# Kernel optimization log

Hardware: AMD Instinct MI355X
Metric: run time of the kernel (lower is better)

## Reference

```python
import jax, jax.numpy as jnp
import numpy as np

N_NODES = 100000
N_EDGES = 1600000
IN_SIZE, HID_SIZE, OUT_SIZE = 128, 64, 64


def _glorot(key, shape):
    lim = float(np.sqrt(6.0 / (shape[0] + shape[1])))
    return jax.random.uniform(key, shape, jnp.float32, -lim, lim)


def setup_inputs() -> dict:
    key = jax.random.key(0)
    ks = jax.random.split(key, 6)
    features = jax.random.normal(ks[0], (N_NODES, IN_SIZE), jnp.float32)
    src = jax.random.randint(ks[1], (N_EDGES,), 0, N_NODES)
    dst = jax.random.randint(ks[2], (N_EDGES,), 0, N_NODES)
    return {
        "features": features,
        "W0": _glorot(ks[3], (IN_SIZE, HID_SIZE)),
        "b0": jnp.zeros((HID_SIZE,), jnp.float32),
        "W1": _glorot(ks[4], (HID_SIZE, HID_SIZE)),
        "b1": jnp.zeros((HID_SIZE,), jnp.float32),
        "W2": _glorot(ks[5], (HID_SIZE, OUT_SIZE)),
        "b2": jnp.zeros((OUT_SIZE,), jnp.float32),
        "src": src,
        "dst": dst,
    }


def reference(features, W0, b0, W1, b1, W2, b2, src, dst):
    # DGL GraphConv with norm='both': h' = relu(D_in^{-1/2} A D_out^{-1/2} h W + b)
    # Dropout layers are identity in eval mode (deterministic baseline).
    N = features.shape[0]
    ones = jnp.ones(src.shape, features.dtype)
    deg_out = jax.ops.segment_sum(ones, src, num_segments=N)
    deg_in = jax.ops.segment_sum(ones, dst, num_segments=N)
    norm_src = jnp.where(deg_out > 0, deg_out, 1.0) ** -0.5  # [N]
    norm_dst = jnp.where(deg_in > 0, deg_in, 1.0) ** -0.5    # [N]

    def layer(h, W, b):
        h = h * norm_src[:, None]          # source-side degree norm
        m = (h @ W)[src]                   # project first (in >= out), then gather [E, d_out]
        agg = jax.ops.segment_sum(m, dst, num_segments=N)  # scatter-add to destinations
        return jax.nn.relu(agg * norm_dst[:, None] + b)

    h = layer(features, W0, b0)
    h = layer(h, W1, b1)
    return layer(h, W2, b2)
```

## Files before the change

### kernel.cpp

```cpp
#include <hip/hip_runtime.h>
#include <hip/hip_bf16.h>

typedef __hip_bfloat16 bf16;
typedef __attribute__((ext_vector_type(8))) short bf16x8;
typedef __attribute__((ext_vector_type(8))) unsigned short u16x8;
typedef __attribute__((ext_vector_type(4))) float f32x4;
typedef __attribute__((ext_vector_type(4))) int i32x4;
typedef __attribute__((ext_vector_type(4))) short s16x4;

__device__ __forceinline__ float b2f(unsigned short u) {
  return __uint_as_float(((unsigned)u) << 16);
}
__device__ __forceinline__ unsigned short f2b(float x) {
  bf16 h = __float2bfloat16(x);
  return *reinterpret_cast<unsigned short*>(&h);
}

__global__ void k_passA(const int* __restrict__ src, const int* __restrict__ dst, int E,
                        int nbuck, int M, int* __restrict__ counts,
                        const unsigned short* __restrict__ raw, int* __restrict__ flag) {
  if (blockIdx.x == 256) {
    __shared__ int sbad, snz;
    const int t = threadIdx.x;
    if (t == 0) { sbad = 0; snz = 0; }
    __syncthreads();
    const unsigned short u = raw[t];
    const float a = fabsf(b2f(u));
    if (!(a < 100.f)) atomicAdd(&sbad, 1);
    if (((t & 1) == 0) && u != 0) atomicAdd(&snz, 1);
    __syncthreads();
    if (t == 0) flag[0] = (sbad == 0 && snz > 0) ? 1 : 0;
    return;
  }
  extern __shared__ int lh[];
  int* lh1 = lh;
  int* lh2 = lh + nbuck;
  const int t = threadIdx.x;
  for (int k = t; k < 2 * nbuck; k += 256) lh[k] = 0;
  __syncthreads();
  const int chunk = (E + 255) / 256;
  const int s = blockIdx.x * chunk;
  const int e = min(E, s + chunk);
  for (int i = s + t; i < e; i += 256) {
    atomicAdd(&lh1[dst[i] >> 8], 1);
    atomicAdd(&lh2[src[i] >> 8], 1);
  }
  __syncthreads();
  for (int k = t; k < nbuck; k += 256) {
    counts[k * 256 + blockIdx.x] = lh1[k];
    counts[M + k * 256 + blockIdx.x] = lh2[k];
  }
}

__global__ void k_scan1(const int* __restrict__ a, int M2, int* __restrict__ bsums) {
  __shared__ int sdata[256];
  int i = blockIdx.x * 256 + threadIdx.x;
  int v = (i < M2) ? a[i] : 0;
  sdata[threadIdx.x] = v;
  __syncthreads();
  for (int s = 128; s > 0; s >>= 1) {
    if (threadIdx.x < s) sdata[threadIdx.x] += sdata[threadIdx.x + s];
    __syncthreads();
  }
  if (threadIdx.x == 0) bsums[blockIdx.x] = sdata[0];
}

__global__ void k_scan2(int* __restrict__ bsums, int nb, int* __restrict__ rowStart,
                        int N, int E) {
  __shared__ int s[1024];
  const int t = threadIdx.x;
  const int v = (t < nb) ? bsums[t] : 0;
  s[t] = v;
  __syncthreads();
  for (int off = 1; off < 1024; off <<= 1) {
    int u = (t >= off) ? s[t - off] : 0;
    __syncthreads();
    s[t] += u;
    __syncthreads();
  }
  if (t < nb) bsums[t] = s[t] - v;
  if (t == 0) rowStart[N] = E;
}

__global__ void k_scan3(int* __restrict__ a, int M2, const int* __restrict__ bsums) {
  __shared__ int sdata[256];
  int i = blockIdx.x * 256 + threadIdx.x;
  int v = (i < M2) ? a[i] : 0;
  sdata[threadIdx.x] = v;
  __syncthreads();
  for (int off = 1; off < 256; off <<= 1) {
    int t = (threadIdx.x >= off) ? sdata[threadIdx.x - off] : 0;
    __syncthreads();
    sdata[threadIdx.x] += t;
    __syncthreads();
  }
  if (i < M2) a[i] = bsums[blockIdx.x] + sdata[threadIdx.x] - v;
}

__global__ void k_passC(const int* __restrict__ src, const int* __restrict__ dst, int E,
                        int nbuck, int M, const int* __restrict__ S,
                        int* __restrict__ tmp, unsigned char* __restrict__ tmp2) {
  extern __shared__ int cur[];
  int* cur1 = cur;
  int* cur2 = cur + nbuck;
  const int t = threadIdx.x;
  for (int k = t; k < nbuck; k += 256) {
    cur1[k] = S[k * 256 + blockIdx.x];
    cur2[k] = S[M + k * 256 + blockIdx.x];
  }
  __syncthreads();
  const int chunk = (E + 255) / 256;
  const int s = blockIdx.x * chunk;
  const int e = min(E, s + chunk);
  for (int i = s + t; i < e; i += 256) {
    const int sv = src[i];
    const int d = dst[i];
    const int pos1 = atomicAdd(&cur1[d >> 8], 1);
    tmp[pos1] = sv | ((d & 255) << 20);
    const int pos2 = atomicAdd(&cur2[sv >> 8], 1);
    tmp2[pos2 - E] = (unsigned char)(sv & 255);
  }
}

__global__ void k_passD(const int* __restrict__ tmp, const unsigned char* __restrict__ tmp2,
                        const int* __restrict__ S, int nbuck, int M, int N, int E,
                        int* __restrict__ rowStart, int* __restrict__ edgeSrc,
                        float* __restrict__ ns, float* __restrict__ nd) {
  __shared__ int h[256];
  __shared__ int ex[256];
  __shared__ int c[256];
  const int t = threadIdx.x;
  const int k = blockIdx.x;
  const int node = k * 256 + t;
  const int bs2 = S[M + k * 256] - E;
  const int be2 = (k + 1 < nbuck) ? (S[M + (k + 1) * 256] - E) : E;
  h[t] = 0;
  __syncthreads();
  for (int i = bs2 + t; i < be2; i += 256) atomicAdd(&h[tmp2[i]], 1);
  __syncthreads();
  if (node < N) {
    int dov = h[t];
    if (dov <= 0) dov = 1;
    ns[node] = rsqrtf((float)dov);
  }
  __syncthreads();
  const int bs = S[k * 256];
  const int be = (k + 1 < nbuck) ? S[(k + 1) * 256] : E;
  h[t] = 0;
  __syncthreads();
  for (int i = bs + t; i < be; i += 256) atomicAdd(&h[tmp[i] >> 20], 1);
  __syncthreads();
  const int cnt = h[t];
  ex[t] = cnt;
  __syncthreads();
  for (int off = 1; off < 256; off <<= 1) {
    int u = (t >= off) ? ex[t - off] : 0;
    __syncthreads();
    ex[t] += u;
    __syncthreads();
  }
  const int excl = ex[t] - cnt;
  if (node < N) {
    rowStart[node] = bs + excl;
    nd[node] = rsqrtf((float)(cnt > 0 ? cnt : 1));
  }
  c[t] = bs + excl;
  __syncthreads();
  for (int i = bs + t; i < be; i += 256) {
    const int v = tmp[i];
    const int pos = atomicAdd(&c[v >> 20], 1);
    edgeSrc[pos] = v & 0xFFFFF;
  }
}

template <int K, bool FIRST, bool SCALE>
__device__ __forceinline__ void gemm_loadA(const void* hin, bool isb, int rowA,
                                           int quad, bf16x8* A) {
  constexpr int KT = K / 32;
  if (FIRST && !isb) {
    const float* hp = (const float*)hin + (size_t)rowA * K;
#pragma unroll
    for (int kt = 0; kt < KT; ++kt) {
      const float4 u0 = *(const float4*)(hp + kt * 32 + quad * 8);
      const float4 u1 = *(const float4*)(hp + kt * 32 + quad * 8 + 4);
      A[kt][0] = (short)f2b(u0.x); A[kt][1] = (short)f2b(u0.y);
      A[kt][2] = (short)f2b(u0.z); A[kt][3] = (short)f2b(u0.w);
      A[kt][4] = (short)f2b(u1.x); A[kt][5] = (short)f2b(u1.y);
      A[kt][6] = (short)f2b(u1.z); A[kt][7] = (short)f2b(u1.w);
    }
  } else {
    const unsigned short* hp = (const unsigned short*)hin + (size_t)rowA * K;
#pragma unroll
    for (int kt = 0; kt < KT; ++kt)
      A[kt] = *(const bf16x8*)(hp + kt * 32 + quad * 8);
  }
}

template <int K, bool FIRST, bool SCALE>
__global__ void __launch_bounds__(256) k_gemm(
    const void* __restrict__ hin, const void* __restrict__ Wv,
    const int* __restrict__ flag, const float* __restrict__ norm_src,
    int N, unsigned short* __restrict__ out) {
  constexpr int KT = K / 32;
  constexpr int ST = K + 8;
  constexpr int CST = 72;
  __shared__ unsigned short Wl[64 * ST];
  __shared__ unsigned short Cl[4][16 * CST];
  const bool isb = (*flag != 0);
  const int tid = threadIdx.x;

  {
    const unsigned short* Wus = (const unsigned short*)Wv;
    const float* Wf = (const float*)Wv;
    for (int i0 = tid * 8; i0 < K * 64; i0 += 2048) {
      const int k = i0 >> 6;
      const int n0 = i0 & 63;
      unsigned short v[8];
      if (isb) {
        const u16x8 u = *(const u16x8*)(Wus + i0);
#pragma unroll
        for (int j = 0; j < 8; ++j) v[j] = u[j];
      } else {
        const float4 f0 = *(const float4*)(Wf + i0);
        const float4 f1 = *(const float4*)(Wf + i0 + 4);
        v[0] = f2b(f0.x); v[1] = f2b(f0.y); v[2] = f2b(f0.z); v[3] = f2b(f0.w);
        v[4] = f2b(f1.x); v[5] = f2b(f1.y); v[6] = f2b(f1.z); v[7] = f2b(f1.w);
      }
#pragma unroll
      for (int j = 0; j < 8; ++j) Wl[(n0 + j) * ST + k] = v[j];
    }
  }
  __syncthreads();

  const int lane = tid & 63;
  const int quad = lane >> 4;
  const int l16 = lane & 15;
  const int w = tid >> 6;
  unsigned short* myC = &Cl[w][0];

  const int wid = blockIdx.x * 4 + w;
  const int nw = gridDim.x * 4;
  const int G = (N + 15) >> 4;

  bf16x8 A0[KT], A1[KT];
  if (wid < G) {
    int r0 = (wid << 4) + l16;
    if (r0 >= N) r0 = N - 1;
    gemm_loadA<K, FIRST, SCALE>(hin, isb, r0, quad, A0);
  }
  for (int g = wid; g < G; g += nw) {
    if (g + nw < G) {
      int r1 = ((g + nw) << 4) + l16;
      if (r1 >= N) r1 = N - 1;
      gemm_loadA<K, FIRST, SCALE>(hin, isb, r1, quad, A1);
    }
    f32x4 acc[4] = {{0.f, 0.f, 0.f, 0.f}, {0.f, 0.f, 0.f, 0.f},
                    {0.f, 0.f, 0.f, 0.f}, {0.f, 0.f, 0.f, 0.f}};
#pragma unroll
    for (int kt = 0; kt < KT; ++kt) {
      const int koff = kt * 32 + quad * 8;
#pragma unroll
      for (int nt = 0; nt < 4; ++nt) {
        const bf16x8 Bf = *(const bf16x8*)&Wl[(nt * 16 + l16) * ST + koff];
        acc[nt] = __builtin_amdgcn_mfma_f32_16x16x32_bf16(A0[kt], Bf, acc[nt], 0, 0, 0);
      }
    }
    const int rowD = quad * 4;
#pragma unroll
    for (int r = 0; r < 4; ++r) {
      const int nodeW = (g << 4) + rowD + r;
      const float f = (SCALE && nodeW < N) ? norm_src[nodeW] : 1.0f;
#pragma unroll
      for (int nt = 0; nt < 4; ++nt)
        myC[(rowD + r) * CST + nt * 16 + l16] = f2b(SCALE ? acc[nt][r] * f : acc[nt][r]);
    }
    const int row2 = lane >> 2;
    const int c0 = (lane & 3) * 16;
    const int node = (g << 4) + row2;
    if (node < N) {
      const u16x8 v0 = *(const u16x8*)&myC[row2 * CST + c0];
      const u16x8 v1 = *(const u16x8*)&myC[row2 * CST + c0 + 8];
      *(u16x8*)(out + (size_t)node * 64 + c0) = v0;
      *(u16x8*)(out + (size_t)node * 64 + c0 + 8) = v1;
    }
#pragma unroll
    for (int kt = 0; kt < KT; ++kt) A0[kt] = A1[kt];
  }
}

__device__ __forceinline__ void agg_chunk_compute(unsigned trbase, int cb32, int lo,
                                                  unsigned span, int quad, f32x4* acc) {
  const int posbase = cb32 + (quad << 2);
  const unsigned u0 = (unsigned)(posbase - lo);
  bf16x8 Af;
#pragma unroll
  for (int j = 0; j < 8; ++j) {
    const unsigned off = (j < 4) ? (unsigned)j : (unsigned)(12 + j);
    Af[j] = ((u0 + off) < span) ? (short)0x3F80 : (short)0;
  }
  s16x4 t0[4], t1[4];
#pragma unroll
  for (int nt = 0; nt < 4; ++nt) {
    const unsigned a = trbase + (unsigned)(nt * 1024);
    asm volatile("ds_read_b64_tr_b16 %0, %1" : "=v"(t0[nt]) : "v"(a) : "memory");
    asm volatile("ds_read_b64_tr_b16 %0, %1 offset:512" : "=v"(t1[nt]) : "v"(a) : "memory");
  }
  asm volatile("s_waitcnt lgkmcnt(0)" ::: "memory");
  __builtin_amdgcn_sched_barrier(0);
#pragma unroll
  for (int nt = 0; nt < 4; ++nt) {
    bf16x8 Bf;
    Bf[0] = t0[nt][0]; Bf[1] = t0[nt][1]; Bf[2] = t0[nt][2]; Bf[3] = t0[nt][3];
    Bf[4] = t1[nt][0]; Bf[5] = t1[nt][1]; Bf[6] = t1[nt][2]; Bf[7] = t1[nt][3];
    acc[nt] = __builtin_amdgcn_mfma_f32_16x16x32_bf16(Af, Bf, acc[nt], 0, 0, 0);
  }
}

template <bool LAST, bool FUSE>
__global__ void __launch_bounds__(256) k_aggregate(
    const unsigned short* __restrict__ proj,
    const int* __restrict__ edgeSrc, const int* __restrict__ rowStart,
    const float* __restrict__ norm_dst, const float* __restrict__ norm_src,
    const void* __restrict__ bias, const int* __restrict__ flag,
    const void* __restrict__ Wv, int N, int E, void* __restrict__ outp) {
  __shared__ unsigned short lds[4][2048];
  const bool isb = (*flag != 0);
  const int tid = threadIdx.x;
  const int w = tid >> 6;
  const int lane = tid & 63;
  const int l16 = lane & 15;
  const int quad = lane >> 4;
  const int e32 = lane & 31;
  const int p = lane >> 5;

  const int wid = blockIdx.x * 4 + w;
  const int g0 = wid * 8;

  float bcol[4];
#pragma unroll
  for (int nt = 0; nt < 4; ++nt) {
    const int col = nt * 16 + l16;
    bcol[nt] = isb ? b2f(((const unsigned short*)bias)[col]) : ((const float*)bias)[col];
  }

  const int cb = rowStart[min(g0, N)];
  const int ce = rowStart[min(g0 + 8, N)];
  const int L = ce - cb;
  const int nch = (L + 31) >> 5;

  const int rsi = min(g0 + min(l16, 8), N);
  const int rsj = min(g0 + min(l16 + 1, 8), N);
  const int lo = rowStart[rsi];
  const unsigned span = (unsigned)(rowStart[rsj] - lo);

  int idxc[6];
#pragma unroll
  for (int t = 0; t < 6; ++t) {
    const int pos = min(cb + t * 32 + e32, E - 1);
    idxc[t] = edgeSrc[pos];
  }

  unsigned short* myl = &lds[w][0];
  unsigned wofs[4];
#pragma unroll
  for (int q = 0; q < 4; ++q) {
    const int n0 = p * 32 + q * 8;
    wofs[q] = (unsigned)((n0 >> 4) * 512 + e32 * 16 + (n0 & 15));
  }
  const unsigned trbase = (unsigned)(uintptr_t)myl + (unsigned)lane * 8u;

  f32x4 acc[4] = {{0.f, 0.f, 0.f, 0.f}, {0.f, 0.f, 0.f, 0.f},
                  {0.f, 0.f, 0.f, 0.f}, {0.f, 0.f, 0.f, 0.f}};

  i32x4 gb[2][4];
#define AGG_ISSUE(t, b)                                                         \
  {                                                                             \
    const unsigned short* rp = proj + (size_t)idxc[t] * 64 + p * 32;            \
    gb[b][0] = *(const i32x4*)(rp);                                             \
    gb[b][1] = *(const i32x4*)(rp + 8);                                         \
    gb[b][2] = *(const i32x4*)(rp + 16);                                        \
    gb[b][3] = *(const i32x4*)(rp + 24);                                        \
  }
  if (0 < nch) AGG_ISSUE(0, 0);
  if (1 < nch) AGG_ISSUE(1, 1);

#pragma unroll
  for (int tt = 0; tt < 6; ++tt) {
    if (tt < nch) {
#pragma unroll
      for (int q = 0; q < 4; ++q) *(i32x4*)(myl + wofs[q]) = gb[tt & 1][q];
      if (tt + 2 < 6 && tt + 2 < nch) AGG_ISSUE(tt + 2, tt & 1);
      asm volatile("s_waitcnt lgkmcnt(0)" ::: "memory");
      agg_chunk_compute(trbase, cb + tt * 32, lo, span, quad, acc);
    }
  }
  for (int t = 6; t < nch; ++t) {
    const int pos = min(cb + t * 32 + e32, E - 1);
    const int idx = edgeSrc[pos];
    const unsigned short* rp = proj + (size_t)idx * 64 + p * 32;
    i32x4 g4[4];
    g4[0] = *(const i32x4*)(rp);
    g4[1] = *(const i32x4*)(rp + 8);
    g4[2] = *(const i32x4*)(rp + 16);
    g4[3] = *(const i32x4*)(rp + 24);
#pragma unroll
    for (int q = 0; q < 4; ++q) *(i32x4*)(myl + wofs[q]) = g4[q];
    asm volatile("s_waitcnt lgkmcnt(0)" ::: "memory");
    agg_chunk_compute(trbase, cb + t * 32, lo, span, quad, acc);
  }
#undef AGG_ISSUE

  if constexpr (FUSE) {
    __shared__ unsigned short hT[32 * 72];
    __shared__ unsigned short Wl2[64 * 72];
    {
      const unsigned short* Wus = (const unsigned short*)Wv;
      const float* Wf = (const float*)Wv;
      for (int i0 = tid * 8; i0 < 64 * 64; i0 += 2048) {
        const int k = i0 >> 6;
        const int n0 = i0 & 63;
        unsigned short v[8];
        if (isb) {
          const u16x8 u = *(const u16x8*)(Wus + i0);
#pragma unroll
          for (int j = 0; j < 8; ++j) v[j] = u[j];
        } else {
          const float4 f0 = *(const float4*)(Wf + i0);
          const float4 f1 = *(const float4*)(Wf + i0 + 4);
          v[0] = f2b(f0.x); v[1] = f2b(f0.y); v[2] = f2b(f0.z); v[3] = f2b(f0.w);
          v[4] = f2b(f1.x); v[5] = f2b(f1.y); v[6] = f2b(f1.z); v[7] = f2b(f1.w);
        }
#pragma unroll
        for (int j = 0; j < 8; ++j) Wl2[(n0 + j) * 72 + k] = v[j];
      }
    }
#pragma unroll
    for (int reg = 0; reg < 4; ++reg) {
      const int row = quad * 4 + reg;
      if (row < 8) {
        const int node = min(g0 + row, N - 1);
        const float nd = norm_dst[node];
        const float esc = norm_src[node];
#pragma unroll
        for (int nt = 0; nt < 4; ++nt) {
          const float x = fmaxf(fmaf(acc[nt][reg], nd, bcol[nt]), 0.f) * esc;
          hT[(w * 8 + row) * 72 + nt * 16 + l16] = f2b(x);
        }
      }
    }
    __syncthreads();
    const int r0 = (w & 1) * 16;
    const int cb2 = (w >> 1) * 32;
    bf16x8 Afr[2], Bfr[2][2];
#pragma unroll
    for (int kt = 0; kt < 2; ++kt) {
      const int koff = kt * 32 + quad * 8;
      Afr[kt] = *(const bf16x8*)&hT[(r0 + l16) * 72 + koff];
#pragma unroll
      for (int nt = 0; nt < 2; ++nt)
        Bfr[kt][nt] = *(const bf16x8*)&Wl2[(cb2 + nt * 16 + l16) * 72 + koff];
    }
    f32x4 acc2[2] = {{0.f, 0.f, 0.f, 0.f}, {0.f, 0.f, 0.f, 0.f}};
#pragma unroll
    for (int kt = 0; kt < 2; ++kt)
#pragma unroll
      for (int nt = 0; nt < 2; ++nt)
        acc2[nt] = __builtin_amdgcn_mfma_f32_16x16x32_bf16(Afr[kt], Bfr[kt][nt], acc2[nt], 0, 0, 0);
    __syncthreads();
#pragma unroll
    for (int nt = 0; nt < 2; ++nt)
#pragma unroll
      for (int reg = 0; reg < 4; ++reg) {
        const int row = r0 + quad * 4 + reg;
        hT[row * 72 + cb2 + nt * 16 + l16] = f2b(acc2[nt][reg]);
      }
    __syncthreads();
    const int row = tid >> 3;
    const int c0 = (tid & 7) * 8;
    const int node = blockIdx.x * 32 + row;
    if (node < N) {
      *(u16x8*)((unsigned short*)outp + (size_t)node * 64 + c0) =
          *(const u16x8*)&hT[row * 72 + c0];
    }
  } else {
    if (!isb) {
      float* fs = (float*)myl;
#pragma unroll
      for (int reg = 0; reg < 4; ++reg) {
        const int row = quad * 4 + reg;
        if (row < 8) {
          const int node = min(g0 + row, N - 1);
          const float nd = norm_dst[node];
#pragma unroll
          for (int nt = 0; nt < 4; ++nt)
            fs[row * 64 + nt * 16 + l16] = fmaxf(fmaf(acc[nt][reg], nd, bcol[nt]), 0.f);
        }
      }
      asm volatile("s_waitcnt lgkmcnt(0)" ::: "memory");
      __builtin_amdgcn_sched_barrier(0);
      const int r = lane >> 3;
      const int c0 = (lane & 7) * 8;
      const int node = g0 + r;
      if (node < N) {
        const float4 v0 = *(const float4*)&fs[r * 64 + c0];
        const float4 v1 = *(const float4*)&fs[r * 64 + c0 + 4];
        float* of = (float*)outp + (size_t)node * 64 + c0;
        *(float4*)of = v0;
        *(float4*)(of + 4) = v1;
      }
    } else {
#pragma unroll
      for (int reg = 0; reg < 4; ++reg) {
        const int row = quad * 4 + reg;
        if (row < 8) {
          const int node = min(g0 + row, N - 1);
          const float nd = norm_dst[node];
#pragma unroll
          for (int nt = 0; nt < 4; ++nt) {
            const float x = fmaxf(fmaf(acc[nt][reg], nd, bcol[nt]), 0.f);
            myl[row * 64 + nt * 16 + l16] = f2b(x);
          }
        }
      }
      asm volatile("s_waitcnt lgkmcnt(0)" ::: "memory");
      __builtin_amdgcn_sched_barrier(0);
      if (lane < 32) {
        const int r = lane >> 2;
        const int c0 = (lane & 3) * 16;
        const int node = g0 + r;
        if (node < N) {
          const u16x8 v0 = *(const u16x8*)&myl[r * 64 + c0];
          const u16x8 v1 = *(const u16x8*)&myl[r * 64 + c0 + 8];
          *(u16x8*)((unsigned short*)outp + (size_t)node * 64 + c0) = v0;
          *(u16x8*)((unsigned short*)outp + (size_t)node * 64 + c0 + 8) = v1;
        }
      }
    }
  }
}

extern "C" void kernel_launch(void* const* d_in, const int* in_sizes, int n_in,
                              void* d_out, int out_size, void* d_ws, size_t ws_size,
                              hipStream_t stream) {
  const void* features = d_in[0];
  const void* W0 = d_in[1];
  const void* b0 = d_in[2];
  const void* W1 = d_in[3];
  const void* b1 = d_in[4];
  const void* W2 = d_in[5];
  const void* b2 = d_in[6];
  const int* src = (const int*)d_in[7];
  const int* dst = (const int*)d_in[8];
  const int N = in_sizes[0] / 128;
  const int E = in_sizes[7];
  const int NBUCK = (N + 255) >> 8;
  const int M = NBUCK * 256;
  const int M2 = 2 * M;

  char* w = (char*)d_ws;
  size_t off = 0;
  auto alloc = [&](size_t bytes) {
    void* p = w + off;
    off = (off + bytes + 255) & ~(size_t)255;
    return p;
  };
  int* flag = (int*)alloc(4);
  int* rowStart = (int*)alloc((size_t)(N + 1) * 4);
  int* counts = (int*)alloc((size_t)M2 * 4);
  int* bsums = (int*)alloc(1024 * 4);
  float* norm_src = (float*)alloc((size_t)N * 4);
  float* norm_dst = (float*)alloc((size_t)N * 4);
  int* tmp = (int*)alloc((size_t)E * 4);
  unsigned char* tmp2 = (unsigned char*)alloc((size_t)E);
  int* edgeSrc = (int*)alloc((size_t)E * 4);
  unsigned short* projA = (unsigned short*)alloc((size_t)N * 64 * 2);
  unsigned short* projB = (unsigned short*)alloc((size_t)N * 64 * 2);

  const size_t lds_nb = (size_t)NBUCK * 2 * 4;
  const int GB = 1024;

  k_passA<<<257, 256, lds_nb, stream>>>(src, dst, E, NBUCK, M, counts,
                                        (const unsigned short*)features, flag);
  const int NB2 = (M2 + 255) / 256;
  k_scan1<<<NB2, 256, 0, stream>>>(counts, M2, bsums);
  k_scan2<<<1, 1024, 0, stream>>>(bsums, NB2, rowStart, N, E);
  k_scan3<<<NB2, 256, 0, stream>>>(counts, M2, bsums);
  k_passC<<<256, 256, lds_nb, stream>>>(src, dst, E, NBUCK, M, counts, tmp, tmp2);
  k_passD<<<NBUCK, 256, 0, stream>>>(tmp, tmp2, counts, NBUCK, M, N, E,
                                     rowStart, edgeSrc, norm_src, norm_dst);

  const int AB = (((N + 7) / 8) + 3) / 4;
  k_gemm<128, true, true><<<GB, 256, 0, stream>>>(features, W0, flag, norm_src, N, projA);
  k_aggregate<false, true><<<AB, 256, 0, stream>>>(projA, edgeSrc, rowStart, norm_dst,
                                                   norm_src, b0, flag, W1, N, E, projB);
  k_aggregate<false, true><<<AB, 256, 0, stream>>>(projB, edgeSrc, rowStart, norm_dst,
                                                   norm_src, b1, flag, W2, N, E, projA);
  k_aggregate<true, false><<<AB, 256, 0, stream>>>(projA, edgeSrc, rowStart, norm_dst,
                                                   norm_src, b2, flag, nullptr, N, E, d_out);
}
```

Baseline: 300.2 us.

## Pretranspose W1/W2 once, reuse agg LDS, fix gemm to two tiles per wave

```diff
diff --git a/kernel.cpp b/kernel.cpp
--- a/kernel.cpp
+++ b/kernel.cpp
@@ -50,6 +50,20 @@
     counts[k * 256 + blockIdx.x] = lh1[k];
     counts[M + k * 256 + blockIdx.x] = lh2[k];
   }
+}
+
+__global__ void k_prepW(const void* __restrict__ W1, const void* __restrict__ W2,
+                        const int* __restrict__ flag,
+                        unsigned short* __restrict__ WT1, unsigned short* __restrict__ WT2) {
+  const bool isb = (*flag != 0);
+  const int i = blockIdx.x * 256 + threadIdx.x;
+  const int j = i & 4095;
+  const int n = j >> 6, k = j & 63;
+  const void* W = (i < 4096) ? W1 : W2;
+  unsigned short* WT = (i < 4096) ? WT1 : WT2;
+  const float v = isb ? b2f(((const unsigned short*)W)[k * 64 + n])
+                      : ((const float*)W)[k * 64 + n];
+  WT[j] = f2b(v);
 }
 
 __global__ void k_scan1(const int* __restrict__ a, int M2, int* __restrict__ bsums) {
@@ -208,6 +222,23 @@
   __shared__ unsigned short Cl[4][16 * CST];
   const bool isb = (*flag != 0);
   const int tid = threadIdx.x;
+  const int lane = tid & 63;
+  const int quad = lane >> 4;
+  const int l16 = lane & 15;
+  const int w = tid >> 6;
+
+  const int wid = blockIdx.x * 4 + w;
+  const int nw = gridDim.x * 4;
+  const int G = (N + 15) >> 4;
+  const int g1 = wid + nw;
+
+  bf16x8 A[2][KT];
+  {
+    const int r0 = min((wid << 4) + l16, N - 1);
+    const int r1 = min((g1 << 4) + l16, N - 1);
+    gemm_loadA<K, FIRST, SCALE>(hin, isb, r0, quad, A[0]);
+    gemm_loadA<K, FIRST, SCALE>(hin, isb, r1, quad, A[1]);
+  }
 
   {
     const unsigned short* Wus = (const unsigned short*)Wv;
@@ -232,28 +263,10 @@
   }
   __syncthreads();
 
-  const int lane = tid & 63;
-  const int quad = lane >> 4;
-  const int l16 = lane & 15;
-  const int w = tid >> 6;
   unsigned short* myC = &Cl[w][0];
-
-  const int wid = blockIdx.x * 4 + w;
-  const int nw = gridDim.x * 4;
-  const int G = (N + 15) >> 4;
-
-  bf16x8 A0[KT], A1[KT];
-  if (wid < G) {
-    int r0 = (wid << 4) + l16;
-    if (r0 >= N) r0 = N - 1;
-    gemm_loadA<K, FIRST, SCALE>(hin, isb, r0, quad, A0);
-  }
-  for (int g = wid; g < G; g += nw) {
-    if (g + nw < G) {
-      int r1 = ((g + nw) << 4) + l16;
-      if (r1 >= N) r1 = N - 1;
-      gemm_loadA<K, FIRST, SCALE>(hin, isb, r1, quad, A1);
-    }
+#pragma unroll
+  for (int gi = 0; gi < 2; ++gi) {
+    const int g = (gi == 0) ? wid : g1;
     f32x4 acc[4] = {{0.f, 0.f, 0.f, 0.f}, {0.f, 0.f, 0.f, 0.f},
                     {0.f, 0.f, 0.f, 0.f}, {0.f, 0.f, 0.f, 0.f}};
 #pragma unroll
@@ -262,18 +275,19 @@
 #pragma unroll
       for (int nt = 0; nt < 4; ++nt) {
         const bf16x8 Bf = *(const bf16x8*)&Wl[(nt * 16 + l16) * ST + koff];
-        acc[nt] = __builtin_amdgcn_mfma_f32_16x16x32_bf16(A0[kt], Bf, acc[nt], 0, 0, 0);
+        acc[nt] = __builtin_amdgcn_mfma_f32_16x16x32_bf16(A[gi][kt], Bf, acc[nt], 0, 0, 0);
       }
     }
     const int rowD = quad * 4;
 #pragma unroll
     for (int r = 0; r < 4; ++r) {
-      const int nodeW = (g << 4) + rowD + r;
-      const float f = (SCALE && nodeW < N) ? norm_src[nodeW] : 1.0f;
+      const int nodeW = min((g << 4) + rowD + r, N - 1);
+      const float f = SCALE ? norm_src[nodeW] : 1.0f;
 #pragma unroll
       for (int nt = 0; nt < 4; ++nt)
         myC[(rowD + r) * CST + nt * 16 + l16] = f2b(SCALE ? acc[nt][r] * f : acc[nt][r]);
     }
+    __builtin_amdgcn_sched_barrier(0);
     const int row2 = lane >> 2;
     const int c0 = (lane & 3) * 16;
     const int node = (g << 4) + row2;
@@ -283,8 +297,6 @@
       *(u16x8*)(out + (size_t)node * 64 + c0) = v0;
       *(u16x8*)(out + (size_t)node * 64 + c0 + 8) = v1;
     }
-#pragma unroll
-    for (int kt = 0; kt < KT; ++kt) A0[kt] = A1[kt];
   }
 }
 
@@ -322,7 +334,7 @@
     const int* __restrict__ edgeSrc, const int* __restrict__ rowStart,
     const float* __restrict__ norm_dst, const float* __restrict__ norm_src,
     const void* __restrict__ bias, const int* __restrict__ flag,
-    const void* __restrict__ Wv, int N, int E, void* __restrict__ outp) {
+    const unsigned short* __restrict__ WT, int N, int E, void* __restrict__ outp) {
   __shared__ unsigned short lds[4][2048];
   const bool isb = (*flag != 0);
   const int tid = threadIdx.x;
@@ -411,28 +423,17 @@
 #undef AGG_ISSUE
 
   if constexpr (FUSE) {
-    __shared__ unsigned short hT[32 * 72];
-    __shared__ unsigned short Wl2[64 * 72];
-    {
-      const unsigned short* Wus = (const unsigned short*)Wv;
-      const float* Wf = (const float*)Wv;
-      for (int i0 = tid * 8; i0 < 64 * 64; i0 += 2048) {
-        const int k = i0 >> 6;
-        const int n0 = i0 & 63;
-        unsigned short v[8];
-        if (isb) {
-          const u16x8 u = *(const u16x8*)(Wus + i0);
-#pragma unroll
-          for (int j = 0; j < 8; ++j) v[j] = u[j];
-        } else {
-          const float4 f0 = *(const float4*)(Wf + i0);
-          const float4 f1 = *(const float4*)(Wf + i0 + 4);
-          v[0] = f2b(f0.x); v[1] = f2b(f0.y); v[2] = f2b(f0.z); v[3] = f2b(f0.w);
-          v[4] = f2b(f1.x); v[5] = f2b(f1.y); v[6] = f2b(f1.z); v[7] = f2b(f1.w);
-        }
-#pragma unroll
-        for (int j = 0; j < 8; ++j) Wl2[(n0 + j) * 72 + k] = v[j];
-      }
+    __syncthreads();
+    unsigned short* hT = &lds[0][0];
+    const int r0 = (w & 1) * 16;
+    const int cb2 = (w >> 1) * 32;
+    bf16x8 Bfr[2][2];
+#pragma unroll
+    for (int kt = 0; kt < 2; ++kt) {
+      const int koff = kt * 32 + quad * 8;
+#pragma unroll
+      for (int nt = 0; nt < 2; ++nt)
+        Bfr[kt][nt] = *(const bf16x8*)(WT + (size_t)(cb2 + nt * 16 + l16) * 64 + koff);
     }
 #pragma unroll
     for (int reg = 0; reg < 4; ++reg) {
@@ -449,17 +450,10 @@
       }
     }
     __syncthreads();
-    const int r0 = (w & 1) * 16;
-    const int cb2 = (w >> 1) * 32;
-    bf16x8 Afr[2], Bfr[2][2];
-#pragma unroll
-    for (int kt = 0; kt < 2; ++kt) {
-      const int koff = kt * 32 + quad * 8;
-      Afr[kt] = *(const bf16x8*)&hT[(r0 + l16) * 72 + koff];
-#pragma unroll
-      for (int nt = 0; nt < 2; ++nt)
-        Bfr[kt][nt] = *(const bf16x8*)&Wl2[(cb2 + nt * 16 + l16) * 72 + koff];
-    }
+    bf16x8 Afr[2];
+#pragma unroll
+    for (int kt = 0; kt < 2; ++kt)
+      Afr[kt] = *(const bf16x8*)&hT[(r0 + l16) * 72 + kt * 32 + quad * 8];
     f32x4 acc2[2] = {{0.f, 0.f, 0.f, 0.f}, {0.f, 0.f, 0.f, 0.f}};
 #pragma unroll
     for (int kt = 0; kt < 2; ++kt)
@@ -575,12 +569,16 @@
   int* edgeSrc = (int*)alloc((size_t)E * 4);
   unsigned short* projA = (unsigned short*)alloc((size_t)N * 64 * 2);
   unsigned short* projB = (unsigned short*)alloc((size_t)N * 64 * 2);
+  unsigned short* WT1 = (unsigned short*)alloc(64 * 64 * 2);
+  unsigned short* WT2 = (unsigned short*)alloc(64 * 64 * 2);
 
   const size_t lds_nb = (size_t)NBUCK * 2 * 4;
-  const int GB = 1024;
+  const int G16 = (N + 15) / 16;
+  const int GB = (G16 + 7) / 8;
 
   k_passA<<<257, 256, lds_nb, stream>>>(src, dst, E, NBUCK, M, counts,
                                         (const unsigned short*)features, flag);
+  k_prepW<<<32, 256, 0, stream>>>(W1, W2, flag, WT1, WT2);
   const int NB2 = (M2 + 255) / 256;
   k_scan1<<<NB2, 256, 0, stream>>>(counts, M2, bsums);
   k_scan2<<<1, 1024, 0, stream>>>(bsums, NB2, rowStart, N, E);
@@ -592,9 +590,9 @@
   const int AB = (((N + 7) / 8) + 3) / 4;
   k_gemm<128, true, true><<<GB, 256, 0, stream>>>(features, W0, flag, norm_src, N, projA);
   k_aggregate<false, true><<<AB, 256, 0, stream>>>(projA, edgeSrc, rowStart, norm_dst,
-                                                   norm_src, b0, flag, W1, N, E, projB);
+                                                   norm_src, b0, flag, WT1, N, E, projB);
   k_aggregate<false, true><<<AB, 256, 0, stream>>>(projB, edgeSrc, rowStart, norm_dst,
-                                                   norm_src, b1, flag, W2, N, E, projA);
+                                                   norm_src, b1, flag, WT2, N, E, projA);
   k_aggregate<true, false><<<AB, 256, 0, stream>>>(projA, edgeSrc, rowStart, norm_dst,
                                                    norm_src, b2, flag, nullptr, N, E, d_out);
 }
```

Measured after the change: 302.8 us. Within noise of the previous version (+0.8%).
